# Performance work log

Measured on AMD Instinct MI355X. Metric: run time of the kernel, lower is better.

Reference implementation:

```python
import jax, jax.numpy as jnp
import numpy as np

H, D = 4, 64          # n_heads, feats_per_head (hidden_size = H*D = 256)
NEG_SLOPE = 0.2       # DGL GATv2Conv default negative_slope

N_GT, N_UBS, N_AG = 100000, 20000, 20000
E_SEEN, E_NEAR = 320000, 160000
F_GT, F_UBS, F_AG = 8, 8, 16
HID = H * D


def _linear_params(key, fan_in, fan_out):
    kw, kb = jax.random.split(key)
    s = 1.0 / np.sqrt(fan_in)
    W = jax.random.uniform(kw, (fan_in, fan_out), jnp.float32, -s, s)
    b = jax.random.uniform(kb, (fan_out,), jnp.float32, -s, s)
    return W, b


def setup_inputs() -> dict:
    key = jax.random.key(0)
    ks = jax.random.split(key, 16)
    inp = {
        'x_gt': jax.random.normal(ks[0], (N_GT, F_GT), jnp.float32),
        'x_ubs': jax.random.normal(ks[1], (N_UBS, F_UBS), jnp.float32),
        'x_agent': jax.random.normal(ks[2], (N_AG, F_AG), jnp.float32),
        'seen_src': jax.random.randint(ks[3], (E_SEEN,), 0, N_GT, jnp.int32),
        'seen_dst': jax.random.randint(ks[4], (E_SEEN,), 0, N_AG, jnp.int32),
        'near_src': jax.random.randint(ks[5], (E_NEAR,), 0, N_UBS, jnp.int32),
        'near_dst': jax.random.randint(ks[6], (E_NEAR,), 0, N_AG, jnp.int32),
    }
    # GATv2Conv 'seen': (gt -> agent)
    inp['Ws_seen'], inp['bs_seen'] = _linear_params(ks[7], F_GT, HID)
    inp['Wd_seen'], inp['bd_seen'] = _linear_params(ks[8], F_AG, HID)
    inp['attn_seen'] = jax.random.normal(ks[9], (H, D), jnp.float32) * 0.1
    inp['Wr_seen'], inp['br_seen'] = _linear_params(ks[10], F_AG, HID)
    # GATv2Conv 'near': (ubs -> agent)
    inp['Ws_near'], inp['bs_near'] = _linear_params(ks[11], F_UBS, HID)
    inp['Wd_near'], inp['bd_near'] = _linear_params(ks[12], F_AG, HID)
    inp['attn_near'] = jax.random.normal(ks[13], (H, D), jnp.float32) * 0.1
    inp['Wr_near'], inp['br_near'] = _linear_params(ks[14], F_AG, HID)
    # aggregation MLP: Linear(2*HID, HID) + ReLU
    inp['W_aggr'], inp['b_aggr'] = _linear_params(ks[15], 2 * HID, HID)
    return inp


def _gatv2(h_src, h_dst, src, dst, Ws, bs, Wd, bd, attn, Wr, br, n_dst):
    # DGL GATv2Conv, bipartite, residual=True, allow_zero_in_degree, ReLU activation
    fs = (h_src @ Ws + bs).reshape(-1, H, D)   # [Ns,H,D]
    fd = (h_dst @ Wd + bd).reshape(-1, H, D)   # [Nd,H,D]
    e = jax.nn.leaky_relu(fs[src] + fd[dst], NEG_SLOPE)     # [E,H,D]
    scores = jnp.einsum('ehd,hd->eh', e, attn)              # [E,H]
    # edge softmax over incoming edges of each dst node
    m = jax.ops.segment_max(scores, dst, num_segments=n_dst)
    m = jnp.where(jnp.isfinite(m), m, 0.0)                  # zero-in-degree guard
    ex = jnp.exp(scores - m[dst])
    denom = jax.ops.segment_sum(ex, dst, num_segments=n_dst)
    alpha = ex / denom[dst]                                 # [E,H]
    rst = jax.ops.segment_sum(alpha[:, :, None] * fs[src], dst, num_segments=n_dst)
    rst = rst + (h_dst @ Wr + br).reshape(-1, H, D)         # residual
    return jax.nn.relu(rst).reshape(n_dst, H * D)


def reference(x_gt, x_ubs, x_agent, seen_src, seen_dst, near_src, near_dst,
              Ws_seen, bs_seen, Wd_seen, bd_seen, attn_seen, Wr_seen, br_seen,
              Ws_near, bs_near, Wd_near, bd_near, attn_near, Wr_near, br_near,
              W_aggr, b_aggr):
    n_ag = x_agent.shape[0]
    x1 = _gatv2(x_gt, x_agent, seen_src, seen_dst,
                Ws_seen, bs_seen, Wd_seen, bd_seen, attn_seen, Wr_seen, br_seen, n_ag)
    x2 = _gatv2(x_ubs, x_agent, near_src, near_dst,
                Ws_near, bs_near, Wd_near, bd_near, attn_near, Wr_near, br_near, n_ag)
    x_out = jnp.concatenate((x1, x2), axis=1)               # [N_ag, 2*HID]
    return jax.nn.relu(x_out @ W_aggr + b_aggr)             # [N_ag, HID]
```

## Files before the change

kernel.cpp:

```cpp
#include <hip/hip_runtime.h>
#include <math.h>

#define NEG 0.2f

typedef short bf16x8 __attribute__((ext_vector_type(8)));
typedef float f32x4  __attribute__((ext_vector_type(4)));
typedef float f32x2  __attribute__((ext_vector_type(2)));

static __device__ __forceinline__ void fma4(float4& d, float s, const float4 w) {
    d.x = fmaf(s, w.x, d.x); d.y = fmaf(s, w.y, d.y);
    d.z = fmaf(s, w.z, d.z); d.w = fmaf(s, w.w, d.w);
}
static __device__ __forceinline__ f32x2 pkfma(f32x2 a, f32x2 b, f32x2 c) {
    return __builtin_elementwise_fma(a, b, c);
}
static __device__ __forceinline__ f32x2 splat2(float x) { return (f32x2){x, x}; }

static __device__ __forceinline__ unsigned short f2bf(float f) {
    unsigned int x = __float_as_uint(f);
    unsigned int r = (x + 0x7FFFu + ((x >> 16) & 1u)) >> 16;
    return (unsigned short)r;
}
static __device__ __forceinline__ float rlane(float v, int l) {
    return __int_as_float(__builtin_amdgcn_readlane(__float_as_int(v), l));
}

#define DPP_ADD(x, ctrl) \
    ((x) + __int_as_float(__builtin_amdgcn_update_dpp( \
        __float_as_int(x), __float_as_int(x), (ctrl), 0xF, 0xF, true)))
static __device__ __forceinline__ float rowsum16(float v) {
    v = DPP_ADD(v, 0xB1);
    v = DPP_ADD(v, 0x4E);
    v = DPP_ADD(v, 0x141);
    v = DPP_ADD(v, 0x140);
    return v;
}

__global__ void k_hist_wt(const int* __restrict__ dst_s, int Es,
                          const int* __restrict__ dst_n, int En,
                          int* __restrict__ deg_s, int* __restrict__ deg_n,
                          const float* __restrict__ W, unsigned short* __restrict__ Wt) {
    int i = blockIdx.x * 256 + threadIdx.x;
    if (i < Es) atomicAdd(&deg_s[dst_s[i]], 1);
    int j = i - Es;
    if (j >= 0 && j < En) atomicAdd(&deg_n[dst_n[j]], 1);
    if (i < 512 * 256) {
        int k = i >> 8, n = i & 255;
        Wt[(size_t)n * 512 + k] = f2bf(W[i]);
    }
}

__global__ __launch_bounds__(1024) void k_scan2(int* a, int na, int* b, int nb) {
    int* p = (blockIdx.x == 0) ? a : b;
    int n  = (blockIdx.x == 0) ? na : nb;
    __shared__ int sums[1024];
    int t = threadIdx.x;
    int C = (n + 1023) >> 10;
    int base = t * C;
    int s = 0;
    for (int j = 0; j < C; ++j) { int i = base + j; if (i < n) s += p[i]; }
    sums[t] = s;
    __syncthreads();
    for (int off = 1; off < 1024; off <<= 1) {
        int v = (t >= off) ? sums[t - off] : 0;
        __syncthreads();
        sums[t] += v;
        __syncthreads();
    }
    int run = (t == 0) ? 0 : sums[t - 1];
    for (int j = 0; j < C; ++j) {
        int i = base + j;
        if (i < n) { int v = p[i]; p[i] = run; run += v; }
    }
}

__global__ void k_scatter(const int* __restrict__ src_s, const int* __restrict__ dst_s, int Es,
                          const int* __restrict__ src_n, const int* __restrict__ dst_n, int En,
                          int* __restrict__ cur_s, int* __restrict__ cur_n,
                          int* __restrict__ csr_s, int* __restrict__ csr_n) {
    int i = blockIdx.x * 256 + threadIdx.x;
    if (i < Es) {
        int pos = atomicAdd(&cur_s[dst_s[i]], 1);
        csr_s[pos] = src_s[i];
    }
    int j = i - Es;
    if (j >= 0 && j < En) {
        int pos = atomicAdd(&cur_n[dst_n[j]], 1);
        csr_n[pos] = src_n[j];
    }
}

__global__ __launch_bounds__(256) void k_gat(
    const float* __restrict__ xsrc_s, const int* __restrict__ pfx_s, const int* __restrict__ csr_s,
    const float* __restrict__ Ws_s, const float* __restrict__ bs_s,
    const float* __restrict__ Wd_s, const float* __restrict__ bd_s,
    const float* __restrict__ at_s,
    const float* __restrict__ Wr_s, const float* __restrict__ br_s,
    const float* __restrict__ xsrc_n, const int* __restrict__ pfx_n, const int* __restrict__ csr_n,
    const float* __restrict__ Ws_n, const float* __restrict__ bs_n,
    const float* __restrict__ Wd_n, const float* __restrict__ bd_n,
    const float* __restrict__ at_n,
    const float* __restrict__ Wr_n, const float* __restrict__ br_n,
    const float* __restrict__ x_ag,
    unsigned short* __restrict__ xcat, int n_dst, int gNs)
{
    const bool seen = (int)blockIdx.x < gNs;
    const float* x_src = seen ? xsrc_s : xsrc_n;
    const int*   pfx   = seen ? pfx_s  : pfx_n;
    const int*   csr   = seen ? csr_s  : csr_n;
    const float* Ws    = seen ? Ws_s   : Ws_n;
    const float* bs    = seen ? bs_s   : bs_n;
    const float* Wd    = seen ? Wd_s   : Wd_n;
    const float* bd    = seen ? bd_s   : bd_n;
    const float* at    = seen ? at_s   : at_n;
    const float* Wr    = seen ? Wr_s   : Wr_n;
    const float* br    = seen ? br_s   : br_n;
    const int col = seen ? 0 : 256;
    const int blk = seen ? (int)blockIdx.x : (int)blockIdx.x - gNs;

    const int t = threadIdx.x;
    const int wave = t >> 6, lane = t & 63;
    const int d0 = lane * 4;

    int gnode = blk * 16 + ((lane >> 4) << 2) + wave;
    int gn = (gnode < n_dst) ? gnode : (n_dst - 1);
    float xag = x_ag[(size_t)gn * 16 + (lane & 15)];

    int e_start[4], e_end[4];
#pragma unroll
    for (int j = 0; j < 4; ++j) {
        int nd = blk * 16 + j * 4 + wave;
        nd = (nd < n_dst) ? nd : (n_dst - 1);
        e_end[j]   = pfx[nd];
        e_start[j] = nd ? pfx[nd - 1] : 0;
    }

    f32x2 fd01[4], fd23[4], fr01[4], fr23[4];
    {
        float4 bdv = *(const float4*)&bd[d0];
        float4 brv = *(const float4*)&br[d0];
#pragma unroll
        for (int j = 0; j < 4; ++j) {
            fd01[j] = (f32x2){bdv.x, bdv.y}; fd23[j] = (f32x2){bdv.z, bdv.w};
            fr01[j] = (f32x2){brv.x, brv.y}; fr23[j] = (f32x2){brv.z, brv.w};
        }
#pragma unroll
        for (int k = 0; k < 16; ++k) {
            float4 wd = *(const float4*)&Wd[k * 256 + d0];
            float4 wr = *(const float4*)&Wr[k * 256 + d0];
            f32x2 wd01 = {wd.x, wd.y}, wd23 = {wd.z, wd.w};
            f32x2 wr01 = {wr.x, wr.y}, wr23 = {wr.z, wr.w};
#pragma unroll
            for (int j = 0; j < 4; ++j) {
                f32x2 xk = splat2(rlane(xag, j * 16 + k));
                fd01[j] = pkfma(xk, wd01, fd01[j]);
                fd23[j] = pkfma(xk, wd23, fd23[j]);
                fr01[j] = pkfma(xk, wr01, fr01[j]);
                fr23[j] = pkfma(xk, wr23, fr23[j]);
            }
        }
    }

    f32x2 ws01[8], ws23[8];
#pragma unroll
    for (int k = 0; k < 8; ++k) {
        float4 w = *(const float4*)&Ws[k * 256 + d0];
        ws01[k] = (f32x2){w.x, w.y};
        ws23[k] = (f32x2){w.z, w.w};
    }
    f32x2 bs01, bs23, at01, at23;
    {
        float4 b4 = *(const float4*)&bs[d0];
        float4 a4 = *(const float4*)&at[d0];
        bs01 = (f32x2){b4.x, b4.y}; bs23 = (f32x2){b4.z, b4.w};
        at01 = (f32x2){a4.x, a4.y}; at23 = (f32x2){a4.z, a4.w};
    }

#pragma unroll
    for (int rep = 0; rep < 4; ++rep) {
        const int node = blk * 16 + rep * 4 + wave;
        if (node >= n_dst) continue;

        const int start = e_start[rep];
        const int deg   = e_end[rep] - start;
        const f32x2 fd01r = fd01[rep], fd23r = fd23[rep];

        float l = 0.f;
        f32x2 a01 = {0.f, 0.f}, a23 = {0.f, 0.f};

        if (deg > 0) {
            const int gs = lane >> 3;
            const int w8 = lane & 7;

            int e0 = (gs < deg) ? gs : deg - 1;
            int i0 = csr[start + e0];
            float r0 = x_src[(size_t)i0 * 8 + w8];
            int e1 = (8 + gs < deg) ? 8 + gs : deg - 1;
            int i1 = csr[start + e1];

            for (int base = 0; base < deg; base += 8) {
                float r1 = x_src[(size_t)i1 * 8 + w8];
                int e2 = base + 16 + gs; e2 = (e2 < deg) ? e2 : deg - 1;
                int i2 = csr[start + e2];

#pragma unroll
                for (int j = 0; j < 8; ++j) {
                    if (base + j < deg) {
                        f32x2 x0 = splat2(rlane(r0, j * 8 + 0));
                        f32x2 x1 = splat2(rlane(r0, j * 8 + 1));
                        f32x2 x2 = splat2(rlane(r0, j * 8 + 2));
                        f32x2 x3 = splat2(rlane(r0, j * 8 + 3));
                        f32x2 x4 = splat2(rlane(r0, j * 8 + 4));
                        f32x2 x5 = splat2(rlane(r0, j * 8 + 5));
                        f32x2 x6 = splat2(rlane(r0, j * 8 + 6));
                        f32x2 x7 = splat2(rlane(r0, j * 8 + 7));

                        f32x2 fs01 = bs01, fs23 = bs23;
                        fs01 = pkfma(x0, ws01[0], fs01); fs23 = pkfma(x0, ws23[0], fs23);
                        fs01 = pkfma(x1, ws01[1], fs01); fs23 = pkfma(x1, ws23[1], fs23);
                        fs01 = pkfma(x2, ws01[2], fs01); fs23 = pkfma(x2, ws23[2], fs23);
                        fs01 = pkfma(x3, ws01[3], fs01); fs23 = pkfma(x3, ws23[3], fs23);
                        fs01 = pkfma(x4, ws01[4], fs01); fs23 = pkfma(x4, ws23[4], fs23);
                        fs01 = pkfma(x5, ws01[5], fs01); fs23 = pkfma(x5, ws23[5], fs23);
                        fs01 = pkfma(x6, ws01[6], fs01); fs23 = pkfma(x6, ws23[6], fs23);
                        fs01 = pkfma(x7, ws01[7], fs01); fs23 = pkfma(x7, ws23[7], fs23);

                        f32x2 t01 = fs01 + fd01r;
                        f32x2 t23 = fs23 + fd23r;
                        t01 = __builtin_elementwise_max(t01, NEG * t01);
                        t23 = __builtin_elementwise_max(t23, NEG * t23);

                        f32x2 scp = t01 * at01;
                        scp = pkfma(t23, at23, scp);
                        float sc = scp.x + scp.y;
                        sc = rowsum16(sc);

                        float p = __expf(sc);
                        l += p;
                        f32x2 pp = splat2(p);
                        a01 = pkfma(pp, fs01, a01);
                        a23 = pkfma(pp, fs23, a23);
                    }
                }
                r0 = r1; i1 = i2;
            }
        }

        float inv = (l > 0.f) ? 1.f / l : 0.f;
        ushort4 o;
        o.x = f2bf(fmaxf(fmaf(a01.x, inv, fr01[rep].x), 0.f));
        o.y = f2bf(fmaxf(fmaf(a01.y, inv, fr01[rep].y), 0.f));
        o.z = f2bf(fmaxf(fmaf(a23.x, inv, fr23[rep].x), 0.f));
        o.w = f2bf(fmaxf(fmaf(a23.y, inv, fr23[rep].y), 0.f));
        *(ushort4*)&xcat[(size_t)node * 512 + col + d0] = o;
    }
}

__global__ __launch_bounds__(256) void k_mlp(
    const unsigned short* __restrict__ X, const unsigned short* __restrict__ Wt,
    const float* __restrict__ b, float* __restrict__ out, int M)
{
    const int t = threadIdx.x;
    const int wave = t >> 6, lane = t & 63;
    const int m16 = lane & 15, q = lane >> 4;
    const int rbase = blockIdx.x * 16;
    const int nbase = wave * 64;

    int rowa = rbase + m16; if (rowa >= M) rowa = M - 1;
    const unsigned short* xp = X + (size_t)rowa * 512 + q * 8;
    const unsigned short* w0 = Wt + (size_t)(nbase + m16) * 512 + q * 8;
    const unsigned short* w1 = w0 + 16 * 512;
    const unsigned short* w2 = w0 + 32 * 512;
    const unsigned short* w3 = w0 + 48 * 512;

    f32x4 ac0 = {0.f, 0.f, 0.f, 0.f}, ac1 = ac0, ac2 = ac0, ac3 = ac0;

#pragma unroll
    for (int k0 = 0; k0 < 512; k0 += 32) {
        bf16x8 a  = *(const bf16x8*)(xp + k0);
        bf16x8 b0 = *(const bf16x8*)(w0 + k0);
        bf16x8 b1 = *(const bf16x8*)(w1 + k0);
        bf16x8 b2 = *(const bf16x8*)(w2 + k0);
        bf16x8 b3 = *(const bf16x8*)(w3 + k0);
        ac0 = __builtin_amdgcn_mfma_f32_16x16x32_bf16(a, b0, ac0, 0, 0, 0);
        ac1 = __builtin_amdgcn_mfma_f32_16x16x32_bf16(a, b1, ac1, 0, 0, 0);
        ac2 = __builtin_amdgcn_mfma_f32_16x16x32_bf16(a, b2, ac2, 0, 0, 0);
        ac3 = __builtin_amdgcn_mfma_f32_16x16x32_bf16(a, b3, ac3, 0, 0, 0);
    }

#define EPI(AC, J) { \
        int coln = nbase + (J) * 16 + m16; \
        float bias = b[coln]; \
        _Pragma("unroll") \
        for (int r = 0; r < 4; ++r) { \
            int orow = rbase + q * 4 + r; \
            if (orow < M) \
                out[(size_t)orow * 256 + coln] = fmaxf(AC[r] + bias, 0.f); \
        } }
    EPI(ac0, 0) EPI(ac1, 1) EPI(ac2, 2) EPI(ac3, 3)
#undef EPI
}

extern "C" void kernel_launch(void* const* d_in, const int* in_sizes, int n_in,
                              void* d_out, int out_size, void* d_ws, size_t ws_size,
                              hipStream_t stream) {
    const float* x_gt   = (const float*)d_in[0];
    const float* x_ubs  = (const float*)d_in[1];
    const float* x_ag   = (const float*)d_in[2];
    const int* seen_src = (const int*)d_in[3];
    const int* seen_dst = (const int*)d_in[4];
    const int* near_src = (const int*)d_in[5];
    const int* near_dst = (const int*)d_in[6];
    const float* Ws_s = (const float*)d_in[7];  const float* bs_s = (const float*)d_in[8];
    const float* Wd_s = (const float*)d_in[9];  const float* bd_s = (const float*)d_in[10];
    const float* at_s = (const float*)d_in[11];
    const float* Wr_s = (const float*)d_in[12]; const float* br_s = (const float*)d_in[13];
    const float* Ws_n = (const float*)d_in[14]; const float* bs_n = (const float*)d_in[15];
    const float* Wd_n = (const float*)d_in[16]; const float* bd_n = (const float*)d_in[17];
    const float* at_n = (const float*)d_in[18];
    const float* Wr_n = (const float*)d_in[19]; const float* br_n = (const float*)d_in[20];
    const float* W_a  = (const float*)d_in[21]; const float* b_a  = (const float*)d_in[22];

    const int n_ag = in_sizes[2] / 16;
    const int E_s  = in_sizes[3];
    const int E_n  = in_sizes[5];

    char* ws = (char*)d_ws;
    int* cur_s = (int*)ws;              ws += (size_t)n_ag * 4;
    int* cur_n = (int*)ws;              ws += (size_t)n_ag * 4;
    int* csr_s = (int*)ws;              ws += (size_t)E_s * 4;
    int* csr_n = (int*)ws;              ws += (size_t)E_n * 4;
    unsigned short* xcat = (unsigned short*)ws;  ws += (size_t)n_ag * 512 * 2;
    unsigned short* Wt   = (unsigned short*)ws;

    hipMemsetAsync(cur_s, 0, (size_t)n_ag * 8, stream);

    int gE = (E_s + E_n + 255) / 256;
    k_hist_wt<<<gE, 256, 0, stream>>>(seen_dst, E_s, near_dst, E_n, cur_s, cur_n, W_a, Wt);
    k_scan2<<<2, 1024, 0, stream>>>(cur_s, n_ag, cur_n, n_ag);
    k_scatter<<<gE, 256, 0, stream>>>(seen_src, seen_dst, E_s, near_src, near_dst, E_n,
                                      cur_s, cur_n, csr_s, csr_n);

    int gN = (n_ag + 15) / 16;
    k_gat<<<2 * gN, 256, 0, stream>>>(
        x_gt,  cur_s, csr_s, Ws_s, bs_s, Wd_s, bd_s, at_s, Wr_s, br_s,
        x_ubs, cur_n, csr_n, Ws_n, bs_n, Wd_n, bd_n, at_n, Wr_n, br_n,
        x_ag, xcat, n_ag, gN);

    k_mlp<<<(n_ag + 15) / 16, 256, 0, stream>>>(xcat, Wt, b_a, (float*)d_out, n_ag);
}
```

Before: 310.5 us.

## Precompute bf16 source projections per node instead of recomputing per edge

Source-feature projections fs = x_src@Ws+bs are now computed once per source node inside the histogram kernel and stored as bf16. The GAT kernel gathers the precomputed 256-wide rows per edge with an 8-deep software prefetch, instead of recomputing an 8x256 matvec for every edge. This cuts per-edge FMA work but makes each edge read 512 bytes instead of 32, and fs is rounded to bf16. The loop also swaps the per-edge branch for masking p to zero.

After: 339.9 us. 9.4% more time.

```diff
diff --git a/kernel.cpp b/kernel.cpp
--- a/kernel.cpp
+++ b/kernel.cpp
@@ -7,10 +7,6 @@
 typedef float f32x4  __attribute__((ext_vector_type(4)));
 typedef float f32x2  __attribute__((ext_vector_type(2)));
 
-static __device__ __forceinline__ void fma4(float4& d, float s, const float4 w) {
-    d.x = fmaf(s, w.x, d.x); d.y = fmaf(s, w.y, d.y);
-    d.z = fmaf(s, w.z, d.z); d.w = fmaf(s, w.w, d.w);
-}
 static __device__ __forceinline__ f32x2 pkfma(f32x2 a, f32x2 b, f32x2 c) {
     return __builtin_elementwise_fma(a, b, c);
 }
@@ -36,10 +32,15 @@
     return v;
 }
 
-__global__ void k_hist_wt(const int* __restrict__ dst_s, int Es,
-                          const int* __restrict__ dst_n, int En,
-                          int* __restrict__ deg_s, int* __restrict__ deg_n,
-                          const float* __restrict__ W, unsigned short* __restrict__ Wt) {
+__global__ void k_hist_wt_fs(
+    const int* __restrict__ dst_s, int Es, const int* __restrict__ dst_n, int En,
+    int* __restrict__ deg_s, int* __restrict__ deg_n,
+    const float* __restrict__ W, unsigned short* __restrict__ Wt,
+    const float* __restrict__ x_s, const float* __restrict__ Ws_s,
+    const float* __restrict__ bs_s, unsigned short* __restrict__ fs_s, int Ns,
+    const float* __restrict__ x_n, const float* __restrict__ Ws_n,
+    const float* __restrict__ bs_n, unsigned short* __restrict__ fs_n, int Nn)
+{
     int i = blockIdx.x * 256 + threadIdx.x;
     if (i < Es) atomicAdd(&deg_s[dst_s[i]], 1);
     int j = i - Es;
@@ -48,6 +49,29 @@
         int k = i >> 8, n = i & 255;
         Wt[(size_t)n * 512 + k] = f2bf(W[i]);
     }
+
+    int wv = i >> 6, lane = i & 63;
+    const float *x, *Ws, *bs; unsigned short* fs; int node;
+    if (wv < Ns)           { x = x_s; Ws = Ws_s; bs = bs_s; fs = fs_s; node = wv; }
+    else if (wv < Ns + Nn) { x = x_n; Ws = Ws_n; bs = bs_n; fs = fs_n; node = wv - Ns; }
+    else return;
+
+    const int d0 = lane * 4;
+    float4 b4 = *(const float4*)&bs[d0];
+    f32x2 a01 = {b4.x, b4.y}, a23 = {b4.z, b4.w};
+    float4 xa = *(const float4*)&x[(size_t)node * 8];
+    float4 xb = *(const float4*)&x[(size_t)node * 8 + 4];
+    float xs[8] = {xa.x, xa.y, xa.z, xa.w, xb.x, xb.y, xb.z, xb.w};
+#pragma unroll
+    for (int k = 0; k < 8; ++k) {
+        float4 w = *(const float4*)&Ws[k * 256 + d0];
+        f32x2 xk = splat2(xs[k]);
+        a01 = pkfma(xk, (f32x2){w.x, w.y}, a01);
+        a23 = pkfma(xk, (f32x2){w.z, w.w}, a23);
+    }
+    ushort4 o;
+    o.x = f2bf(a01.x); o.y = f2bf(a01.y); o.z = f2bf(a23.x); o.w = f2bf(a23.y);
+    *(ushort4*)&fs[(size_t)node * 256 + d0] = o;
 }
 
 __global__ __launch_bounds__(1024) void k_scan2(int* a, int na, int* b, int nb) {
@@ -91,13 +115,11 @@
 }
 
 __global__ __launch_bounds__(256) void k_gat(
-    const float* __restrict__ xsrc_s, const int* __restrict__ pfx_s, const int* __restrict__ csr_s,
-    const float* __restrict__ Ws_s, const float* __restrict__ bs_s,
+    const unsigned short* __restrict__ fsrc_s, const int* __restrict__ pfx_s, const int* __restrict__ csr_s,
     const float* __restrict__ Wd_s, const float* __restrict__ bd_s,
     const float* __restrict__ at_s,
     const float* __restrict__ Wr_s, const float* __restrict__ br_s,
-    const float* __restrict__ xsrc_n, const int* __restrict__ pfx_n, const int* __restrict__ csr_n,
-    const float* __restrict__ Ws_n, const float* __restrict__ bs_n,
+    const unsigned short* __restrict__ fsrc_n, const int* __restrict__ pfx_n, const int* __restrict__ csr_n,
     const float* __restrict__ Wd_n, const float* __restrict__ bd_n,
     const float* __restrict__ at_n,
     const float* __restrict__ Wr_n, const float* __restrict__ br_n,
@@ -105,11 +127,9 @@
     unsigned short* __restrict__ xcat, int n_dst, int gNs)
 {
     const bool seen = (int)blockIdx.x < gNs;
-    const float* x_src = seen ? xsrc_s : xsrc_n;
+    const unsigned short* fsrc = seen ? fsrc_s : fsrc_n;
     const int*   pfx   = seen ? pfx_s  : pfx_n;
     const int*   csr   = seen ? csr_s  : csr_n;
-    const float* Ws    = seen ? Ws_s   : Ws_n;
-    const float* bs    = seen ? bs_s   : bs_n;
     const float* Wd    = seen ? Wd_s   : Wd_n;
     const float* bd    = seen ? bd_s   : bd_n;
     const float* at    = seen ? at_s   : at_n;
@@ -161,18 +181,9 @@
         }
     }
 
-    f32x2 ws01[8], ws23[8];
-#pragma unroll
-    for (int k = 0; k < 8; ++k) {
-        float4 w = *(const float4*)&Ws[k * 256 + d0];
-        ws01[k] = (f32x2){w.x, w.y};
-        ws23[k] = (f32x2){w.z, w.w};
-    }
-    f32x2 bs01, bs23, at01, at23;
+    f32x2 at01, at23;
     {
-        float4 b4 = *(const float4*)&bs[d0];
         float4 a4 = *(const float4*)&at[d0];
-        bs01 = (f32x2){b4.x, b4.y}; bs23 = (f32x2){b4.z, b4.w};
         at01 = (f32x2){a4.x, a4.y}; at23 = (f32x2){a4.z, a4.w};
     }
 
@@ -189,60 +200,60 @@
         f32x2 a01 = {0.f, 0.f}, a23 = {0.f, 0.f};
 
         if (deg > 0) {
-            const int gs = lane >> 3;
-            const int w8 = lane & 7;
-
-            int e0 = (gs < deg) ? gs : deg - 1;
-            int i0 = csr[start + e0];
-            float r0 = x_src[(size_t)i0 * 8 + w8];
-            int e1 = (8 + gs < deg) ? 8 + gs : deg - 1;
-            int i1 = csr[start + e1];
+            int iN[8];
+            uint2 fC[8];
+#pragma unroll
+            for (int j = 0; j < 8; ++j) {
+                int e = (j < deg) ? j : deg - 1;
+                iN[j] = csr[start + e];
+            }
+#pragma unroll
+            for (int j = 0; j < 8; ++j)
+                fC[j] = *(const uint2*)&fsrc[(((unsigned)iN[j]) << 8) | (unsigned)d0];
+#pragma unroll
+            for (int j = 0; j < 8; ++j) {
+                int e = 8 + j; e = (e < deg) ? e : deg - 1;
+                iN[j] = csr[start + e];
+            }
 
             for (int base = 0; base < deg; base += 8) {
-                float r1 = x_src[(size_t)i1 * 8 + w8];
-                int e2 = base + 16 + gs; e2 = (e2 < deg) ? e2 : deg - 1;
-                int i2 = csr[start + e2];
-
+                uint2 fN[8]; int iN2[8];
+#pragma unroll
+                for (int j = 0; j < 8; ++j)
+                    fN[j] = *(const uint2*)&fsrc[(((unsigned)iN[j]) << 8) | (unsigned)d0];
 #pragma unroll
                 for (int j = 0; j < 8; ++j) {
-                    if (base + j < deg) {
-                        f32x2 x0 = splat2(rlane(r0, j * 8 + 0));
-                        f32x2 x1 = splat2(rlane(r0, j * 8 + 1));
-                        f32x2 x2 = splat2(rlane(r0, j * 8 + 2));
-                        f32x2 x3 = splat2(rlane(r0, j * 8 + 3));
-                        f32x2 x4 = splat2(rlane(r0, j * 8 + 4));
-                        f32x2 x5 = splat2(rlane(r0, j * 8 + 5));
-                        f32x2 x6 = splat2(rlane(r0, j * 8 + 6));
-                        f32x2 x7 = splat2(rlane(r0, j * 8 + 7));
-
-                        f32x2 fs01 = bs01, fs23 = bs23;
-                        fs01 = pkfma(x0, ws01[0], fs01); fs23 = pkfma(x0, ws23[0], fs23);
-                        fs01 = pkfma(x1, ws01[1], fs01); fs23 = pkfma(x1, ws23[1], fs23);
-                        fs01 = pkfma(x2, ws01[2], fs01); fs23 = pkfma(x2, ws23[2], fs23);
-                        fs01 = pkfma(x3, ws01[3], fs01); fs23 = pkfma(x3, ws23[3], fs23);
-                        fs01 = pkfma(x4, ws01[4], fs01); fs23 = pkfma(x4, ws23[4], fs23);
-                        fs01 = pkfma(x5, ws01[5], fs01); fs23 = pkfma(x5, ws23[5], fs23);
-                        fs01 = pkfma(x6, ws01[6], fs01); fs23 = pkfma(x6, ws23[6], fs23);
-                        fs01 = pkfma(x7, ws01[7], fs01); fs23 = pkfma(x7, ws23[7], fs23);
-
-                        f32x2 t01 = fs01 + fd01r;
-                        f32x2 t23 = fs23 + fd23r;
-                        t01 = __builtin_elementwise_max(t01, NEG * t01);
-                        t23 = __builtin_elementwise_max(t23, NEG * t23);
-
-                        f32x2 scp = t01 * at01;
-                        scp = pkfma(t23, at23, scp);
-                        float sc = scp.x + scp.y;
-                        sc = rowsum16(sc);
-
-                        float p = __expf(sc);
-                        l += p;
-                        f32x2 pp = splat2(p);
-                        a01 = pkfma(pp, fs01, a01);
-                        a23 = pkfma(pp, fs23, a23);
-                    }
+                    int e = base + 16 + j; e = (e < deg) ? e : deg - 1;
+                    iN2[j] = csr[start + e];
                 }
-                r0 = r1; i1 = i2;
+#pragma unroll
+                for (int j = 0; j < 8; ++j) {
+                    unsigned lo = fC[j].x, hi = fC[j].y;
+                    f32x2 fs01, fs23;
+                    fs01.x = __uint_as_float(lo << 16);
+                    fs01.y = __uint_as_float(lo & 0xffff0000u);
+                    fs23.x = __uint_as_float(hi << 16);
+                    fs23.y = __uint_as_float(hi & 0xffff0000u);
+
+                    f32x2 t01 = fs01 + fd01r;
+                    f32x2 t23 = fs23 + fd23r;
+                    t01 = __builtin_elementwise_max(t01, NEG * t01);
+                    t23 = __builtin_elementwise_max(t23, NEG * t23);
+
+                    f32x2 scp = t01 * at01;
+                    scp = pkfma(t23, at23, scp);
+                    float sc = scp.x + scp.y;
+                    sc = rowsum16(sc);
+
+                    float p = __expf(sc);
+                    p = (base + j < deg) ? p : 0.f;
+                    l += p;
+                    f32x2 pp = splat2(p);
+                    a01 = pkfma(pp, fs01, a01);
+                    a23 = pkfma(pp, fs23, a23);
+                }
+#pragma unroll
+                for (int j = 0; j < 8; ++j) { fC[j] = fN[j]; iN[j] = iN2[j]; }
             }
         }
 
@@ -324,6 +335,8 @@
     const int n_ag = in_sizes[2] / 16;
     const int E_s  = in_sizes[3];
     const int E_n  = in_sizes[5];
+    const int Ns   = in_sizes[0] / 8;
+    const int Nn   = in_sizes[1] / 8;
 
     char* ws = (char*)d_ws;
     int* cur_s = (int*)ws;              ws += (size_t)n_ag * 4;
@@ -331,20 +344,27 @@
     int* csr_s = (int*)ws;              ws += (size_t)E_s * 4;
     int* csr_n = (int*)ws;              ws += (size_t)E_n * 4;
     unsigned short* xcat = (unsigned short*)ws;  ws += (size_t)n_ag * 512 * 2;
-    unsigned short* Wt   = (unsigned short*)ws;
+    unsigned short* Wt   = (unsigned short*)ws;  ws += (size_t)512 * 256 * 2;
+    unsigned short* fs_s = (unsigned short*)ws;  ws += (size_t)Ns * 256 * 2;
+    unsigned short* fs_n = (unsigned short*)ws;
 
     hipMemsetAsync(cur_s, 0, (size_t)n_ag * 8, stream);
 
     int gE = (E_s + E_n + 255) / 256;
-    k_hist_wt<<<gE, 256, 0, stream>>>(seen_dst, E_s, near_dst, E_n, cur_s, cur_n, W_a, Wt);
+    int gH = (Ns + Nn + 3) / 4;
+    if (gH < gE) gH = gE;
+    k_hist_wt_fs<<<gH, 256, 0, stream>>>(seen_dst, E_s, near_dst, E_n, cur_s, cur_n,
+                                         W_a, Wt,
+                                         x_gt,  Ws_s, bs_s, fs_s, Ns,
+                                         x_ubs, Ws_n, bs_n, fs_n, Nn);
     k_scan2<<<2, 1024, 0, stream>>>(cur_s, n_ag, cur_n, n_ag);
     k_scatter<<<gE, 256, 0, stream>>>(seen_src, seen_dst, E_s, near_src, near_dst, E_n,
                                       cur_s, cur_n, csr_s, csr_n);
 
     int gN = (n_ag + 15) / 16;
     k_gat<<<2 * gN, 256, 0, stream>>>(
-        x_gt,  cur_s, csr_s, Ws_s, bs_s, Wd_s, bd_s, at_s, Wr_s, br_s,
-        x_ubs, cur_n, csr_n, Ws_n, bs_n, Wd_n, bd_n, at_n, Wr_n, br_n,
+        fs_s, cur_s, csr_s, Wd_s, bd_s, at_s, Wr_s, br_s,
+        fs_n, cur_n, csr_n, Wd_n, bd_n, at_n, Wr_n, br_n,
         x_ag, xcat, n_ag, gN);
 
     k_mlp<<<(n_ag + 15) / 16, 256, 0, stream>>>(xcat, Wt, b_a, (float*)d_out, n_ag);
```

## Flatten per-node edge loops into one pipelined chunk stream across nodes

Applied to the files above, without the earlier changes.

Replaces the four separate per-node edge loops with a single loop over 8-edge chunks that walks across the wave's four destination nodes. This keeps the index and feature prefetch pipeline running across node boundaries, and the first gathers are issued before the Wd/Wr projection work so they overlap it. Per-edge validity branches become predication that zeroes p, and accumulators are kept per node and selected by the node index. The cost is extra select logic and register pressure from four accumulator sets, plus wasted lanes on partial chunks.

Result: slower. 335.7 us (+8.1%).

```diff
diff --git a/kernel.cpp b/kernel.cpp
--- a/kernel.cpp
+++ b/kernel.cpp
@@ -7,10 +7,6 @@
 typedef float f32x4  __attribute__((ext_vector_type(4)));
 typedef float f32x2  __attribute__((ext_vector_type(2)));
 
-static __device__ __forceinline__ void fma4(float4& d, float s, const float4 w) {
-    d.x = fmaf(s, w.x, d.x); d.y = fmaf(s, w.y, d.y);
-    d.z = fmaf(s, w.z, d.z); d.w = fmaf(s, w.w, d.w);
-}
 static __device__ __forceinline__ f32x2 pkfma(f32x2 a, f32x2 b, f32x2 c) {
     return __builtin_elementwise_fma(a, b, c);
 }
@@ -121,18 +117,44 @@
     const int t = threadIdx.x;
     const int wave = t >> 6, lane = t & 63;
     const int d0 = lane * 4;
+    const int gs = lane >> 3;
+    const int w8 = lane & 7;
 
     int gnode = blk * 16 + ((lane >> 4) << 2) + wave;
     int gn = (gnode < n_dst) ? gnode : (n_dst - 1);
     float xag = x_ag[(size_t)gn * 16 + (lane & 15)];
 
-    int e_start[4], e_end[4];
-#pragma unroll
-    for (int j = 0; j < 4; ++j) {
-        int nd = blk * 16 + j * 4 + wave;
-        nd = (nd < n_dst) ? nd : (n_dst - 1);
-        e_end[j]   = pfx[nd];
-        e_start[j] = nd ? pfx[nd - 1] : 0;
+    int st0, st1, st2, st3, dg0, dg1, dg2, dg3;
+    {
+        int nd0 = blk * 16 + 0 * 4 + wave; nd0 = (nd0 < n_dst) ? nd0 : n_dst - 1;
+        int nd1 = blk * 16 + 1 * 4 + wave; nd1 = (nd1 < n_dst) ? nd1 : n_dst - 1;
+        int nd2 = blk * 16 + 2 * 4 + wave; nd2 = (nd2 < n_dst) ? nd2 : n_dst - 1;
+        int nd3 = blk * 16 + 3 * 4 + wave; nd3 = (nd3 < n_dst) ? nd3 : n_dst - 1;
+        int e0 = pfx[nd0], e1 = pfx[nd1], e2 = pfx[nd2], e3 = pfx[nd3];
+        st0 = nd0 ? pfx[nd0 - 1] : 0;
+        st1 = nd1 ? pfx[nd1 - 1] : 0;
+        st2 = nd2 ? pfx[nd2 - 1] : 0;
+        st3 = nd3 ? pfx[nd3 - 1] : 0;
+        dg0 = e0 - st0; dg1 = e1 - st1; dg2 = e2 - st2; dg3 = e3 - st3;
+    }
+
+#define DEG(r)  ((r) == 0 ? dg0 : ((r) == 1 ? dg1 : ((r) == 2 ? dg2 : dg3)))
+#define STRT(r) ((r) == 0 ? st0 : ((r) == 1 ? st1 : ((r) == 2 ? st2 : st3)))
+#define ADV(r, b) { b += 8; if (b >= DEG(r)) { b = 0; ++r; \
+        if (r < 4 && DEG(r) == 0) ++r; \
+        if (r < 4 && DEG(r) == 0) ++r; \
+        if (r < 4 && DEG(r) == 0) ++r; } }
+
+    int ra = 0, ba = 0;
+    if (DEG(ra) == 0) ++ra;
+    if (ra < 4 && DEG(ra) == 0) ++ra;
+    if (ra < 4 && DEG(ra) == 0) ++ra;
+    if (ra < 4 && DEG(ra) == 0) ++ra;
+    int ia = 0;
+    if (ra < 4) {
+        int dg = DEG(ra);
+        int e = ba + gs; e = (e < dg) ? e : dg - 1;
+        ia = csr[STRT(ra) + e];
     }
 
     f32x2 fd01[4], fd23[4], fr01[4], fr23[4];
@@ -161,6 +183,17 @@
         }
     }
 
+    int rb = ra, bb = ba;
+    if (rb < 4) ADV(rb, bb);
+    float xa = 0.f;
+    if (ra < 4) xa = x_src[(size_t)ia * 8 + w8];
+    int ib = 0;
+    if (rb < 4) {
+        int dg = DEG(rb);
+        int e = bb + gs; e = (e < dg) ? e : dg - 1;
+        ib = csr[STRT(rb) + e];
+    }
+
     f32x2 ws01[8], ws23[8];
 #pragma unroll
     for (int k = 0; k < 8; ++k) {
@@ -176,84 +209,98 @@
         at01 = (f32x2){a4.x, a4.y}; at23 = (f32x2){a4.z, a4.w};
     }
 
-#pragma unroll
-    for (int rep = 0; rep < 4; ++rep) {
-        const int node = blk * 16 + rep * 4 + wave;
-        if (node >= n_dst) continue;
-
-        const int start = e_start[rep];
-        const int deg   = e_end[rep] - start;
-        const f32x2 fd01r = fd01[rep], fd23r = fd23[rep];
-
-        float l = 0.f;
-        f32x2 a01 = {0.f, 0.f}, a23 = {0.f, 0.f};
-
-        if (deg > 0) {
-            const int gs = lane >> 3;
-            const int w8 = lane & 7;
-
-            int e0 = (gs < deg) ? gs : deg - 1;
-            int i0 = csr[start + e0];
-            float r0 = x_src[(size_t)i0 * 8 + w8];
-            int e1 = (8 + gs < deg) ? 8 + gs : deg - 1;
-            int i1 = csr[start + e1];
-
-            for (int base = 0; base < deg; base += 8) {
-                float r1 = x_src[(size_t)i1 * 8 + w8];
-                int e2 = base + 16 + gs; e2 = (e2 < deg) ? e2 : deg - 1;
-                int i2 = csr[start + e2];
-
-#pragma unroll
-                for (int j = 0; j < 8; ++j) {
-                    if (base + j < deg) {
-                        f32x2 x0 = splat2(rlane(r0, j * 8 + 0));
-                        f32x2 x1 = splat2(rlane(r0, j * 8 + 1));
-                        f32x2 x2 = splat2(rlane(r0, j * 8 + 2));
-                        f32x2 x3 = splat2(rlane(r0, j * 8 + 3));
-                        f32x2 x4 = splat2(rlane(r0, j * 8 + 4));
-                        f32x2 x5 = splat2(rlane(r0, j * 8 + 5));
-                        f32x2 x6 = splat2(rlane(r0, j * 8 + 6));
-                        f32x2 x7 = splat2(rlane(r0, j * 8 + 7));
-
-                        f32x2 fs01 = bs01, fs23 = bs23;
-                        fs01 = pkfma(x0, ws01[0], fs01); fs23 = pkfma(x0, ws23[0], fs23);
-                        fs01 = pkfma(x1, ws01[1], fs01); fs23 = pkfma(x1, ws23[1], fs23);
-                        fs01 = pkfma(x2, ws01[2], fs01); fs23 = pkfma(x2, ws23[2], fs23);
-                        fs01 = pkfma(x3, ws01[3], fs01); fs23 = pkfma(x3, ws23[3], fs23);
-                        fs01 = pkfma(x4, ws01[4], fs01); fs23 = pkfma(x4, ws23[4], fs23);
-                        fs01 = pkfma(x5, ws01[5], fs01); fs23 = pkfma(x5, ws23[5], fs23);
-                        fs01 = pkfma(x6, ws01[6], fs01); fs23 = pkfma(x6, ws23[6], fs23);
-                        fs01 = pkfma(x7, ws01[7], fs01); fs23 = pkfma(x7, ws23[7], fs23);
-
-                        f32x2 t01 = fs01 + fd01r;
-                        f32x2 t23 = fs23 + fd23r;
-                        t01 = __builtin_elementwise_max(t01, NEG * t01);
-                        t23 = __builtin_elementwise_max(t23, NEG * t23);
-
-                        f32x2 scp = t01 * at01;
-                        scp = pkfma(t23, at23, scp);
-                        float sc = scp.x + scp.y;
-                        sc = rowsum16(sc);
-
-                        float p = __expf(sc);
-                        l += p;
-                        f32x2 pp = splat2(p);
-                        a01 = pkfma(pp, fs01, a01);
-                        a23 = pkfma(pp, fs23, a23);
-                    }
-                }
-                r0 = r1; i1 = i2;
-            }
+    float L0 = 0.f, L1 = 0.f, L2 = 0.f, L3 = 0.f;
+    f32x2 A010 = {0.f, 0.f}, A230 = {0.f, 0.f};
+    f32x2 A011 = {0.f, 0.f}, A231 = {0.f, 0.f};
+    f32x2 A012 = {0.f, 0.f}, A232 = {0.f, 0.f};
+    f32x2 A013 = {0.f, 0.f}, A233 = {0.f, 0.f};
+
+    while (ra < 4) {
+        int rc = rb, bc = bb;
+        if (rc < 4) ADV(rc, bc);
+        float xb = 0.f;
+        if (rb < 4) xb = x_src[(size_t)ib * 8 + w8];
+        int ic = 0;
+        if (rc < 4) {
+            int dg = DEG(rc);
+            int e = bc + gs; e = (e < dg) ? e : dg - 1;
+            ic = csr[STRT(rc) + e];
         }
 
-        float inv = (l > 0.f) ? 1.f / l : 0.f;
-        ushort4 o;
-        o.x = f2bf(fmaxf(fmaf(a01.x, inv, fr01[rep].x), 0.f));
-        o.y = f2bf(fmaxf(fmaf(a01.y, inv, fr01[rep].y), 0.f));
-        o.z = f2bf(fmaxf(fmaf(a23.x, inv, fr23[rep].x), 0.f));
-        o.w = f2bf(fmaxf(fmaf(a23.y, inv, fr23[rep].y), 0.f));
-        *(ushort4*)&xcat[(size_t)node * 512 + col + d0] = o;
-    }
+        const int dga = DEG(ra);
+        const f32x2 fd01c = (ra == 0) ? fd01[0] : ((ra == 1) ? fd01[1] : ((ra == 2) ? fd01[2] : fd01[3]));
+        const f32x2 fd23c = (ra == 0) ? fd23[0] : ((ra == 1) ? fd23[1] : ((ra == 2) ? fd23[2] : fd23[3]));
+
+        float cll = 0.f;
+        f32x2 cl01 = {0.f, 0.f}, cl23 = {0.f, 0.f};
+#pragma unroll
+        for (int j = 0; j < 8; ++j) {
+            f32x2 x0 = splat2(rlane(xa, j * 8 + 0));
+            f32x2 x1 = splat2(rlane(xa, j * 8 + 1));
+            f32x2 x2 = splat2(rlane(xa, j * 8 + 2));
+            f32x2 x3 = splat2(rlane(xa, j * 8 + 3));
+            f32x2 x4 = splat2(rlane(xa, j * 8 + 4));
+            f32x2 x5 = splat2(rlane(xa, j * 8 + 5));
+            f32x2 x6 = splat2(rlane(xa, j * 8 + 6));
+            f32x2 x7 = splat2(rlane(xa, j * 8 + 7));
+
+            f32x2 fs01 = bs01, fs23 = bs23;
+            fs01 = pkfma(x0, ws01[0], fs01); fs23 = pkfma(x0, ws23[0], fs23);
+            fs01 = pkfma(x1, ws01[1], fs01); fs23 = pkfma(x1, ws23[1], fs23);
+            fs01 = pkfma(x2, ws01[2], fs01); fs23 = pkfma(x2, ws23[2], fs23);
+            fs01 = pkfma(x3, ws01[3], fs01); fs23 = pkfma(x3, ws23[3], fs23);
+            fs01 = pkfma(x4, ws01[4], fs01); fs23 = pkfma(x4, ws23[4], fs23);
+            fs01 = pkfma(x5, ws01[5], fs01); fs23 = pkfma(x5, ws23[5], fs23);
+            fs01 = pkfma(x6, ws01[6], fs01); fs23 = pkfma(x6, ws23[6], fs23);
+            fs01 = pkfma(x7, ws01[7], fs01); fs23 = pkfma(x7, ws23[7], fs23);
+
+            f32x2 t01 = fs01 + fd01c;
+            f32x2 t23 = fs23 + fd23c;
+            t01 = __builtin_elementwise_max(t01, NEG * t01);
+            t23 = __builtin_elementwise_max(t23, NEG * t23);
+
+            f32x2 scp = t01 * at01;
+            scp = pkfma(t23, at23, scp);
+            float sc = scp.x + scp.y;
+            sc = rowsum16(sc);
+
+            float p = __expf(sc);
+            p = (ba + j < dga) ? p : 0.f;
+            cll += p;
+            f32x2 pp = splat2(p);
+            cl01 = pkfma(pp, fs01, cl01);
+            cl23 = pkfma(pp, fs23, cl23);
+        }
+
+        if (ra == 0)      { L0 += cll; A010 += cl01; A230 += cl23; }
+        else if (ra == 1) { L1 += cll; A011 += cl01; A231 += cl23; }
+        else if (ra == 2) { L2 += cll; A012 += cl01; A232 += cl23; }
+        else              { L3 += cll; A013 += cl01; A233 += cl23; }
+
+        ra = rb; ba = bb; xa = xb;
+        rb = rc; bb = bc; ib = ic;
+    }
+
+#undef ADV
+#undef STRT
+#undef DEG
+
+#define OUTR(R, LR, A01R, A23R) { \
+        int node = blk * 16 + (R) * 4 + wave; \
+        if (node < n_dst) { \
+            float inv = ((LR) > 0.f) ? 1.f / (LR) : 0.f; \
+            ushort4 o; \
+            o.x = f2bf(fmaxf(fmaf(A01R.x, inv, fr01[R].x), 0.f)); \
+            o.y = f2bf(fmaxf(fmaf(A01R.y, inv, fr01[R].y), 0.f)); \
+            o.z = f2bf(fmaxf(fmaf(A23R.x, inv, fr23[R].x), 0.f)); \
+            o.w = f2bf(fmaxf(fmaf(A23R.y, inv, fr23[R].y), 0.f)); \
+            *(ushort4*)&xcat[(size_t)node * 512 + col + d0] = o; \
+        } }
+    OUTR(0, L0, A010, A230)
+    OUTR(1, L1, A011, A231)
+    OUTR(2, L2, A012, A232)
+    OUTR(3, L3, A013, A233)
+#undef OUTR
 }
 
 __global__ __launch_bounds__(256) void k_mlp(
```
